# Performance work log

Hardware: AMD Instinct MI355X
Metric: run time of the kernel (lower is better)

The kernel has to match this reference:

```python
import jax, jax.numpy as jnp
import numpy as np

H1 = 768
H2 = 768
B, LQ, LK = 8, 1024, 1024


def setup_inputs() -> dict:
    key = jax.random.key(0)
    ks = jax.random.split(key, 12)
    s1 = 1.0 / np.sqrt(H1)
    s2 = 1.0 / np.sqrt(H2)
    # weights stored as [in, out] (equivalent to torch Linear weight.T)
    return {
        "tensor1": jax.random.normal(ks[0], (B, LQ, H1), jnp.float32),
        "tensor2": jax.random.normal(ks[1], (B, LK, H2), jnp.float32),
        "Wq": jax.random.uniform(ks[2], (3, H1, H2), jnp.float32, -s1, s1),
        "bq": jax.random.uniform(ks[3], (3, H2), jnp.float32, -s1, s1),
        "Wk": jax.random.uniform(ks[4], (3, H2, H2), jnp.float32, -s2, s2),
        "bk": jax.random.uniform(ks[5], (3, H2), jnp.float32, -s2, s2),
        "Wv": jax.random.uniform(ks[6], (3, H2, H2), jnp.float32, -s2, s2),
        "bv": jax.random.uniform(ks[7], (3, H2), jnp.float32, -s2, s2),
        "Wp": jax.random.uniform(ks[8], (3 * H2, H2), jnp.float32, -1.0 / np.sqrt(3 * H2), 1.0 / np.sqrt(3 * H2)),
        "bp": jax.random.uniform(ks[9], (H2,), jnp.float32, -1.0 / np.sqrt(3 * H2), 1.0 / np.sqrt(3 * H2)),
    }


def reference(tensor1, tensor2, Wq, bq, Wk, bk, Wv, bv, Wp, bp):
    # Three independent cross-attention heads, stacked on leading axis h=3.
    q = jnp.einsum("bqd,hde->hbqe", tensor1, Wq) + bq[:, None, None, :]  # [3,B,LQ,H2]
    k = jnp.einsum("bkd,hde->hbke", tensor2, Wk) + bk[:, None, None, :]  # [3,B,LK,H2]
    v = jnp.einsum("bkd,hde->hbke", tensor2, Wv) + bv[:, None, None, :]  # [3,B,LK,H2]
    scores = jnp.einsum("hbqe,hbke->hbqk", q, k)  # NOTE: no 1/sqrt(d) scaling, per original
    weights = jax.nn.softmax(scores, axis=-1)
    ctx = jnp.einsum("hbqk,hbke->hbqe", weights, v)  # [3,B,LQ,H2]
    # concat heads along feature dim -> [B,LQ,3*H2]
    multi = jnp.transpose(ctx, (1, 2, 0, 3)).reshape(ctx.shape[1], ctx.shape[2], -1)
    # project_multihead: ReLU then Linear
    return jax.nn.relu(multi) @ Wp + bp
```

## Files before the change

### kernel.cpp

```cpp
#include <hip/hip_runtime.h>
#include <hip/hip_bf16.h>


typedef _Float16 f16;
typedef __attribute__((ext_vector_type(8))) _Float16 f16x8;
typedef __attribute__((ext_vector_type(4))) float f32x4;
typedef __attribute__((ext_vector_type(4))) short s16x4;

#define DI __device__ __forceinline__

DI short f2hs(float f){
  f16 h = (f16)f;
  return __builtin_bit_cast(short, h);
}
DI float hs2f(short s){
  return (float)__builtin_bit_cast(f16, s);
}

DI f32x4 mfma16(f16x8 a, f16x8 b, f32x4 c){
  return __builtin_amdgcn_mfma_f32_16x16x32_f16(a, b, c, 0, 0, 0);
}

#define GLL16(gp, lp) __builtin_amdgcn_global_load_lds( \
    (const __attribute__((address_space(1))) unsigned int*)(gp), \
    (__attribute__((address_space(3))) unsigned int*)(lp), 16, 0, 0)

__global__ void cvt2_f16_kernel(const float* __restrict__ a, const float* __restrict__ b,
                                short* __restrict__ oa, short* __restrict__ ob, int n4each){
  int i = blockIdx.x * blockDim.x + threadIdx.x;
  const float* in = (i < n4each) ? a : b;
  short* out = (i < n4each) ? oa : ob;
  int j = (i < n4each) ? i : i - n4each;
  f32x4 v = ((const f32x4*)in)[j];
  s16x4 o;
  o[0]=f2hs(v[0]); o[1]=f2hs(v[1]); o[2]=f2hs(v[2]); o[3]=f2hs(v[3]);
  ((s16x4*)out)[j] = o;
}

__global__ void transpose2_kernel(const float* __restrict__ Wv, const float* __restrict__ Wp,
                                  short* __restrict__ WvT, short* __restrict__ WpT){
  __shared__ float tile[32][33];
  const float* in; short* out; int R, r0;
  if (blockIdx.z == 0){
    int hd = blockIdx.y / 24;
    in = Wv + (long)hd*768*768; out = WvT + (long)hd*768*768;
    R = 768; r0 = (blockIdx.y % 24) * 32;
  } else {
    in = Wp; out = WpT; R = 2304; r0 = blockIdx.y * 32;
  }
  int c0 = blockIdx.x * 32;
  int tx = threadIdx.x, ty = threadIdx.y;
  #pragma unroll
  for (int k=0;k<4;k++)
    tile[ty + k*8][tx] = in[(long)(r0 + ty + k*8) * 768 + c0 + tx];
  __syncthreads();
  #pragma unroll
  for (int k=0;k<4;k++)
    out[(long)(c0 + ty + k*8) * R + r0 + tx] = f2hs(tile[tx][ty + k*8]);
}

DI void gemm_tile64(const short* __restrict__ A, const short* __restrict__ Bt, int K,
                    int m0, int n0, short* As, short* Bs, f32x4 (&acc)[4][4])
{
  const int tid = threadIdx.x, wave = tid>>6, lane = tid&63;
  const int wm = wave>>1, wn = wave&1;
  const int fl = lane&15, fq = lane>>4;
  const int srow = lane>>2, scol = (lane&3)*8;
  for (int kk=0; kk<K; kk+=64){
    __syncthreads();
    #pragma unroll
    for (int c=0;c<2;c++)
      #pragma unroll
      for (int r=0;r<2;r++){
        const int rb = r*64 + wave*16;
        GLL16(A  + (long)(m0+rb+srow)*K + kk + c*32 + scol, As + c*4096 + rb*32);
        GLL16(Bt + (long)(n0+rb+srow)*K + kk + c*32 + scol, Bs + c*4096 + rb*32);
      }
    __syncthreads();
    #pragma unroll
    for (int c=0;c<2;c++){
      f16x8 a[4];
      #pragma unroll
      for (int i=0;i<4;i++) a[i] = *(const f16x8*)(As + c*4096 + (wm*64+i*16+fl)*32 + fq*8);
      #pragma unroll
      for (int j=0;j<4;j++){
        f16x8 b = *(const f16x8*)(Bs + c*4096 + (wn*64+j*16+fl)*32 + fq*8);
        #pragma unroll
        for (int i=0;i<4;i++) acc[i][j] = mfma16(a[i], b, acc[i][j]);
      }
    }
  }
}

__global__ __launch_bounds__(256,2) void gemm_m_kernel(
    const short* __restrict__ WqH, const short* __restrict__ WkH, short* __restrict__ Mt)
{
  __shared__ short As[8192];
  __shared__ short Bs[8192];
  const int h = blockIdx.z;
  const int m0 = blockIdx.x*128, n0 = blockIdx.y*128;
  const int tid = threadIdx.x, wave = tid>>6, lane = tid&63;
  const int wm = wave>>1, wn = wave&1;
  const int fl = lane&15, fq = lane>>4;

  f32x4 vz = {0.f,0.f,0.f,0.f};
  f32x4 acc[4][4];
  #pragma unroll
  for (int i=0;i<4;i++)
    #pragma unroll
    for (int j=0;j<4;j++) acc[i][j] = vz;

  gemm_tile64(WqH + (long)h*768*768, WkH + (long)h*768*768, 768, m0, n0, As, Bs, acc);

  short* outp = Mt + (long)h*768*768;
  #pragma unroll
  for (int j=0;j<4;j++){
    int col = n0 + wn*64 + j*16 + fl;
    #pragma unroll
    for (int i=0;i<4;i++){
      int row = m0 + wm*64 + i*16 + fq*4;
      s16x4 pack;
      #pragma unroll
      for (int r=0;r<4;r++) pack[r] = f2hs(acc[i][j][r]);
      *(s16x4*)(outp + (long)col*768 + row) = pack;
    }
  }
}

__global__ void vvec_kernel(const float* __restrict__ Wk, const float* __restrict__ bq,
                            float* __restrict__ w){
  const int h = blockIdx.x, chunk = blockIdx.y;
  const int tid = threadIdx.x, wave = tid>>6, lane = tid&63;
  const float* bql = bq + h*768 + lane*12;
  float bv[12];
  #pragma unroll
  for (int e=0;e<12;e++) bv[e] = bql[e];
  for (int r = 0; r < 24; r++){
    int d = chunk*96 + r*4 + wave;
    const float* row = Wk + ((long)h*768 + d)*768 + lane*12;
    float s = 0.f;
    #pragma unroll
    for (int e=0;e<12;e++) s += row[e] * bv[e];
    s += __shfl_xor(s, 1);
    s += __shfl_xor(s, 2);
    s += __shfl_xor(s, 4);
    s += __shfl_xor(s, 8);
    s += __shfl_xor(s, 16);
    s += __shfl_xor(s, 32);
    if (lane == 0) w[h*768 + d] = s;
  }
}

__global__ __launch_bounds__(512,2) void gemm_gv256_kernel(
    const short* __restrict__ t1b, const short* __restrict__ t2b,
    const short* __restrict__ Mt, const short* __restrict__ WvT,
    const float* __restrict__ wv, const float* __restrict__ bv,
    short* __restrict__ Gb, short* __restrict__ Vtb)
{
  __shared__ short As4[4][8192];
  __shared__ short Bs4[4][8192];

  const int z = blockIdx.z;
  const int h = z % 3, which = z / 3;
  const short* A  = (which==0) ? t1b : t2b;
  const short* Bt = ((which==0)?Mt:WvT) + (long)h*768*768;
  const int m0 = blockIdx.x*256, n0 = blockIdx.y*256;
  const int tid = threadIdx.x, wave = tid>>6, lane = tid&63;
  const int wm = wave>>2, wn = wave&3;
  const int fl = lane&15, fq = lane>>4;

  const int lr = lane>>2;
  const int ss = ((lane&3) ^ ((lane>>3)&3)) * 8;
  const int rs = (fq ^ ((fl>>1)&3)) * 8;

  f32x4 vz = {0.f,0.f,0.f,0.f};
  f32x4 acc[8][4];
  #pragma unroll
  for (int i=0;i<8;i++)
    #pragma unroll
    for (int j=0;j<4;j++) acc[i][j] = vz;

  auto STAGE = [&](int rg, int s){
    const int kk = s*32;
    #pragma unroll
    for (int g=0; g<2; g++){
      const int rb = g*128 + wave*16;
      GLL16(A  + (long)(m0+rb+lr)*768 + kk + ss, &As4[rg][rb*32]);
      GLL16(Bt + (long)(n0+rb+lr)*768 + kk + ss, &Bs4[rg][rb*32]);
    }
  };

  auto COMPUTE = [&](int rg){
    const short* Ab = &As4[rg][0];
    const short* Bb = &Bs4[rg][0];
    f16x8 b[4];
    #pragma unroll
    for (int j=0;j<4;j++)
      b[j] = *(const f16x8*)(Bb + (wn*64 + j*16 + fl)*32 + rs);
    #pragma unroll
    for (int mq=0; mq<2; mq++){
      f16x8 a[4];
      #pragma unroll
      for (int i=0;i<4;i++)
        a[i] = *(const f16x8*)(Ab + (wm*128 + mq*64 + i*16 + fl)*32 + rs);
      __builtin_amdgcn_s_setprio(1);
      #pragma unroll
      for (int j=0;j<4;j++)
        #pragma unroll
        for (int i=0;i<4;i++)
          acc[mq*4+i][j] = mfma16(a[i], b[j], acc[mq*4+i][j]);
      __builtin_amdgcn_s_setprio(0);
    }
  };

  STAGE(0, 0);
  STAGE(1, 1);
  asm volatile("s_waitcnt vmcnt(4)" ::: "memory");
  __builtin_amdgcn_s_barrier();

  for (int s = 0; s < 22; ++s){
    STAGE((s+2)&3, s+2);
    asm volatile("s_waitcnt vmcnt(8)" ::: "memory");
    __builtin_amdgcn_s_barrier();
    COMPUTE(s&3);
  }
  asm volatile("s_waitcnt vmcnt(4)" ::: "memory");
  __builtin_amdgcn_s_barrier();
  COMPUTE(22&3);
  asm volatile("s_waitcnt vmcnt(0)" ::: "memory");
  __builtin_amdgcn_s_barrier();
  COMPUTE(23&3);

  if (which == 0){
    const float* bias = wv + h*768;
    short* outp = Gb + (long)h*8192*768;
    #pragma unroll
    for (int j=0;j<4;j++){
      int col = n0 + wn*64 + j*16 + fl;
      float bb = bias[col];
      #pragma unroll
      for (int i=0;i<8;i++){
        int row = m0 + wm*128 + i*16 + fq*4;
        #pragma unroll
        for (int r=0;r<4;r++)
          outp[(long)(row+r)*768 + col] = f2hs(acc[i][j][r] + bb);
      }
    }
  } else {
    const float* bias = bv + h*768;
    const int bidx = m0 >> 10;
    const int lk0  = m0 & 1023;
    short* outp = Vtb + (long)(h*8 + bidx)*768*1024;
    #pragma unroll
    for (int j=0;j<4;j++){
      int e = n0 + wn*64 + j*16 + fl;
      float bb = bias[e];
      #pragma unroll
      for (int i=0;i<8;i++){
        int lk = lk0 + wm*128 + i*16 + fq*4;
        s16x4 pack;
        #pragma unroll
        for (int r=0;r<4;r++) pack[r] = f2hs(acc[i][j][r] + bb);
        *(s16x4*)(outp + (long)e*1024 + lk) = pack;
      }
    }
  }
}

__global__ __launch_bounds__(256,2) void qk_exp_kernel(
    const short* __restrict__ Gb, const short* __restrict__ t2b,
    short* __restrict__ P, float* __restrict__ Mx, float* __restrict__ Lx)
{
  __shared__ short As[8192];
  __shared__ short Bs[8192];
  __shared__ float red0[2][2][64];
  __shared__ float red1[2][2][64];
  const int id = blockIdx.x;
  const int xcd = id & 7, s_ = id >> 3;
  const int hb = xcd*3 + (s_ >> 6);
  const int inner = s_ & 63;
  const int qt = inner & 7, ct = inner >> 3;
  const int h = hb >> 3, b = hb & 7;
  const int tid = threadIdx.x, wave = tid>>6, lane = tid&63;
  const int wm = wave>>1, wn = wave&1;
  const int fl = lane&15, fq = lane>>4;
  const short* Abase = Gb + ((long)h*8192 + b*1024)*768;
  const short* Bbase = t2b + (long)b*1024*768;

  f32x4 vz = {0.f,0.f,0.f,0.f};
  f32x4 acc[4][4];
  #pragma unroll
  for (int i=0;i<4;i++)
    #pragma unroll
    for (int j=0;j<4;j++) acc[i][j] = vz;

  gemm_tile64(Abase, Bbase, 768, qt*128, ct*128, As, Bs, acc);

  float mt[4][4];
  #pragma unroll
  for (int i=0;i<4;i++)
    #pragma unroll
    for (int r=0;r<4;r++){
      float m = acc[i][0][r];
      #pragma unroll
      for (int j=1;j<4;j++) m = fmaxf(m, acc[i][j][r]);
      m = fmaxf(m, __shfl_xor(m, 1));
      m = fmaxf(m, __shfl_xor(m, 2));
      m = fmaxf(m, __shfl_xor(m, 4));
      m = fmaxf(m, __shfl_xor(m, 8));
      mt[i][r] = m;
      if (fl == 0) red0[wn][wm][i*16 + fq*4 + r] = m;
    }
  __syncthreads();
  #pragma unroll
  for (int i=0;i<4;i++)
    #pragma unroll
    for (int r=0;r<4;r++)
      mt[i][r] = fmaxf(red0[0][wm][i*16 + fq*4 + r], red0[1][wm][i*16 + fq*4 + r]);

  #pragma unroll
  for (int i=0;i<4;i++)
    #pragma unroll
    for (int r=0;r<4;r++){
      float s = 0.f;
      #pragma unroll
      for (int j=0;j<4;j++){
        float p = __expf(acc[i][j][r] - mt[i][r]);
        acc[i][j][r] = p;
        s += p;
      }
      s += __shfl_xor(s, 1);
      s += __shfl_xor(s, 2);
      s += __shfl_xor(s, 4);
      s += __shfl_xor(s, 8);
      if (fl == 0) red1[wn][wm][i*16 + fq*4 + r] = s;
    }
  __syncthreads();

  #pragma unroll
  for (int j=0;j<4;j++){
    int c = ct*128 + wn*64 + j*16 + fl;
    #pragma unroll
    for (int i=0;i<4;i++){
      int q = qt*128 + wm*64 + i*16 + fq*4;
      #pragma unroll
      for (int r=0;r<4;r++)
        P[((long)hb*1024 + q + r)*1024 + c] = f2hs(acc[i][j][r]);
    }
  }
  if (fl == 0 && wn == 0){
    long aux = ((long)(hb*8 + ct))*1024 + qt*128;
    #pragma unroll
    for (int i=0;i<4;i++)
      #pragma unroll
      for (int r=0;r<4;r++){
        int row = wm*64 + i*16 + fq*4 + r;
        Mx[aux + row] = mt[i][r];
        Lx[aux + row] = red1[0][wm][row & 63] + red1[1][wm][row & 63];
      }
  }
}

__global__ __launch_bounds__(256,2) void pv_kernel(
    const short* __restrict__ P, const short* __restrict__ Vtb,
    const float* __restrict__ Mx, const float* __restrict__ Lx, short* __restrict__ multi)
{
  __shared__ short As[8192];
  __shared__ short Bs[8192];
  __shared__ float scl[8][128];
  const int id = blockIdx.x;
  const int xcd = id & 7, s_ = id >> 3;
  const int hb = xcd*3 + s_/48;
  const int inner = s_ % 48;
  const int qt = inner & 7, et = inner >> 3;
  const int h = hb >> 3, b = hb & 7;
  const int tid = threadIdx.x, wave = tid>>6, lane = tid&63;
  const int wm = wave>>1, wn = wave&1;
  const int fl = lane&15, fq = lane>>4;
  const int srow = lane>>2, scol = (lane&3)*8;
  const short* Abase = P + (long)hb*1024*1024 + (long)(qt*128)*1024;
  const short* Bbase = Vtb + (long)hb*768*1024 + (long)(et*128)*1024;

  if (tid < 128){
    long a0 = ((long)(hb*8))*1024 + qt*128 + tid;
    float m[8], l[8];
    #pragma unroll
    for (int t=0;t<8;t++){ m[t] = Mx[a0 + t*1024]; l[t] = Lx[a0 + t*1024]; }
    float mg = m[0];
    #pragma unroll
    for (int t=1;t<8;t++) mg = fmaxf(mg, m[t]);
    float lg = 0.f;
    #pragma unroll
    for (int t=0;t<8;t++) lg += l[t] * __expf(m[t] - mg);
    float inv = 1.0f / lg;
    #pragma unroll
    for (int t=0;t<8;t++) scl[t][tid] = __expf(m[t] - mg) * inv;
  }
  __syncthreads();

  f32x4 vz = {0.f,0.f,0.f,0.f};
  f32x4 acc[4][4];
  #pragma unroll
  for (int i=0;i<4;i++)
    #pragma unroll
    for (int j=0;j<4;j++) acc[i][j] = vz;

  for (int ct=0; ct<8; ct++){
    f16 s[4];
    #pragma unroll
    for (int i=0;i<4;i++) s[i] = (f16)scl[ct][wm*64 + i*16 + fl];
    #pragma unroll
    for (int t=0;t<2;t++){
      const int kk = ct*128 + t*64;
      __syncthreads();
      #pragma unroll
      for (int c=0;c<2;c++)
        #pragma unroll
        for (int r=0;r<2;r++){
          const int rb = r*64 + wave*16;
          GLL16(Abase + (long)(rb+srow)*1024 + kk + c*32 + scol, As + c*4096 + rb*32);
          GLL16(Bbase + (long)(rb+srow)*1024 + kk + c*32 + scol, Bs + c*4096 + rb*32);
        }
      __syncthreads();
      #pragma unroll
      for (int c=0;c<2;c++){
        f16x8 a[4];
        #pragma unroll
        for (int i=0;i<4;i++){
          f16x8 av = *(const f16x8*)(As + c*4096 + (wm*64+i*16+fl)*32 + fq*8);
          f16x8 sv;
          #pragma unroll
          for (int e=0;e<8;e++) sv[e] = s[i];
          a[i] = av * sv;
        }
        #pragma unroll
        for (int j=0;j<4;j++){
          f16x8 bvv = *(const f16x8*)(Bs + c*4096 + (wn*64+j*16+fl)*32 + fq*8);
          #pragma unroll
          for (int i=0;i<4;i++) acc[i][j] = mfma16(a[i], bvv, acc[i][j]);
        }
      }
    }
  }

  short* mp = multi + (long)(b*1024 + qt*128)*2304 + h*768 + et*128;
  #pragma unroll
  for (int j=0;j<4;j++){
    int e = wn*64 + j*16 + fl;
    #pragma unroll
    for (int i=0;i<4;i++){
      int q = wm*64 + i*16 + fq*4;
      #pragma unroll
      for (int r=0;r<4;r++)
        mp[(long)(q+r)*2304 + e] = f2hs(fmaxf(acc[i][j][r], 0.f));
    }
  }
}

__global__ __launch_bounds__(256,2) void gemm_out_kernel(
    const short* __restrict__ A, const short* __restrict__ Bt,
    const float* __restrict__ bias, float* __restrict__ out)
{
  __shared__ short As[8192];
  __shared__ short Bs[8192];
  const int m0 = blockIdx.x*128, n0 = blockIdx.y*128;
  const int tid = threadIdx.x, wave = tid>>6, lane = tid&63;
  const int wm = wave>>1, wn = wave&1;
  const int fl = lane&15, fq = lane>>4;

  f32x4 vz = {0.f,0.f,0.f,0.f};
  f32x4 acc[4][4];
  #pragma unroll
  for (int i=0;i<4;i++)
    #pragma unroll
    for (int j=0;j<4;j++) acc[i][j] = vz;

  gemm_tile64(A, Bt, 2304, m0, n0, As, Bs, acc);

  #pragma unroll
  for (int j=0;j<4;j++){
    int col = n0 + wn*64 + j*16 + fl;
    float bb = bias[col];
    #pragma unroll
    for (int i=0;i<4;i++){
      int row = m0 + wm*64 + i*16 + fq*4;
      #pragma unroll
      for (int r=0;r<4;r++)
        out[(long)(row+r)*768 + col] = acc[i][j][r] + bb;
    }
  }
}

extern "C" void kernel_launch(void* const* d_in, const int* in_sizes, int n_in,
                              void* d_out, int out_size, void* d_ws, size_t ws_size,
                              hipStream_t stream)
{
  const float* t1 = (const float*)d_in[0];
  const float* t2 = (const float*)d_in[1];
  const float* Wq = (const float*)d_in[2];
  const float* bq = (const float*)d_in[3];
  const float* Wk = (const float*)d_in[4];
  const float* Wv = (const float*)d_in[6];
  const float* bv = (const float*)d_in[7];
  const float* Wp = (const float*)d_in[8];
  const float* bp = (const float*)d_in[9];
  float* out = (float*)d_out;

  char* ws = (char*)d_ws;
  size_t off = 0;
  auto carve = [&](size_t bytes){ void* p = ws + off; off += (bytes + 255) & ~(size_t)255; return p; };
  short* t1b = (short*)carve(8L*1024*768*2);
  short* t2b = (short*)carve(8L*1024*768*2);
  short* WqH = (short*)carve(3L*768*768*2);
  short* WkH = (short*)carve(3L*768*768*2);
  short* WvT = (short*)carve(3L*768*768*2);
  short* WpT = (short*)carve(768L*2304*2);
  short* Mt  = (short*)carve(3L*768*768*2);
  short* Gb  = (short*)carve(3L*8192*768*2);
  short* Vtb = (short*)carve(3L*8*768*1024*2);
  short* Pb  = (short*)carve(24L*1024*1024*2);
  float* Mx  = (float*)carve(24L*8*1024*4);
  float* Lx  = (float*)carve(24L*8*1024*4);
  float* wvb = (float*)carve(3L*768*4);
  short* multib = Gb;

  cvt2_f16_kernel<<<12288, 256, 0, stream>>>(t1, t2, t1b, t2b, 1572864);
  cvt2_f16_kernel<<<3456, 256, 0, stream>>>(Wq, Wk, WqH, WkH, 442368);
  transpose2_kernel<<<dim3(24,72,2), dim3(32,8), 0, stream>>>(Wv, Wp, WvT, WpT);
  vvec_kernel<<<dim3(3,8), 256, 0, stream>>>(Wk, bq, wvb);
  gemm_m_kernel<<<dim3(6,6,3), 256, 0, stream>>>(WqH, WkH, Mt);
  gemm_gv256_kernel<<<dim3(32,3,6), 512, 0, stream>>>(t1b, t2b, Mt, WvT, wvb, bv, Gb, Vtb);
  qk_exp_kernel<<<1536, 256, 0, stream>>>(Gb, t2b, Pb, Mx, Lx);
  pv_kernel<<<1152, 256, 0, stream>>>(Pb, Vtb, Mx, Lx, multib);
  gemm_out_kernel<<<dim3(64,6,1), 256, 0, stream>>>(multib, WpT, bp, out);
}
```

Before: 413.3 us.

## Deepen GEMM prefetch pipeline with register double-buffered fragments and merged head grid

The G/V projection GEMM now treats the three heads as one wide N dimension (grid 32x9x2 instead of 32x3x6) and precomputes base global pointers. The main loop is restructured to keep three stages of LDS loads in flight instead of two. LDS fragment reads for the next step are double-buffered in registers and issued after the MFMA block, so LDS latency overlaps compute with a single barrier per k-step. The aim is to hide memory and LDS latency better, at the cost of more VGPR pressure from the extra fragment buffers and a fully unrolled loop.

```diff
diff --git a/kernel.cpp b/kernel.cpp
--- a/kernel.cpp
+++ b/kernel.cpp
@@ -151,7 +151,7 @@
   }
 }
 
-__global__ __launch_bounds__(512,2) void gemm_gv256_kernel(
+__global__ __launch_bounds__(512,2) void gemm_gv2_kernel(
     const short* __restrict__ t1b, const short* __restrict__ t2b,
     const short* __restrict__ Mt, const short* __restrict__ WvT,
     const float* __restrict__ wv, const float* __restrict__ bv,
@@ -160,10 +160,9 @@
   __shared__ short As4[4][8192];
   __shared__ short Bs4[4][8192];
 
-  const int z = blockIdx.z;
-  const int h = z % 3, which = z / 3;
-  const short* A  = (which==0) ? t1b : t2b;
-  const short* Bt = ((which==0)?Mt:WvT) + (long)h*768*768;
+  const int which = blockIdx.z;
+  const short* A  = which ? t2b : t1b;
+  const short* Bt = which ? WvT : Mt;
   const int m0 = blockIdx.x*256, n0 = blockIdx.y*256;
   const int tid = threadIdx.x, wave = tid>>6, lane = tid&63;
   const int wm = wave>>2, wn = wave&3;
@@ -173,6 +172,9 @@
   const int ss = ((lane&3) ^ ((lane>>3)&3)) * 8;
   const int rs = (fq ^ ((fl>>1)&3)) * 8;
 
+  const short* Agl = A  + (long)(m0+lr)*768 + ss;
+  const short* Bgl = Bt + (long)(n0+lr)*768 + ss;
+
   f32x4 vz = {0.f,0.f,0.f,0.f};
   f32x4 acc[8][4];
   #pragma unroll
@@ -180,87 +182,95 @@
     #pragma unroll
     for (int j=0;j<4;j++) acc[i][j] = vz;
 
-  auto STAGE = [&](int rg, int s){
+  auto STAGE = [&](int sl, int s){
     const int kk = s*32;
     #pragma unroll
     for (int g=0; g<2; g++){
       const int rb = g*128 + wave*16;
-      GLL16(A  + (long)(m0+rb+lr)*768 + kk + ss, &As4[rg][rb*32]);
-      GLL16(Bt + (long)(n0+rb+lr)*768 + kk + ss, &Bs4[rg][rb*32]);
+      GLL16(Agl + (long)rb*768 + kk, &As4[sl][rb*32]);
+      GLL16(Bgl + (long)rb*768 + kk, &Bs4[sl][rb*32]);
     }
   };
 
-  auto COMPUTE = [&](int rg){
-    const short* Ab = &As4[rg][0];
-    const short* Bb = &Bs4[rg][0];
-    f16x8 b[4];
-    #pragma unroll
-    for (int j=0;j<4;j++)
-      b[j] = *(const f16x8*)(Bb + (wn*64 + j*16 + fl)*32 + rs);
-    #pragma unroll
-    for (int mq=0; mq<2; mq++){
-      f16x8 a[4];
-      #pragma unroll
-      for (int i=0;i<4;i++)
-        a[i] = *(const f16x8*)(Ab + (wm*128 + mq*64 + i*16 + fl)*32 + rs);
-      __builtin_amdgcn_s_setprio(1);
-      #pragma unroll
-      for (int j=0;j<4;j++)
-        #pragma unroll
-        for (int i=0;i<4;i++)
-          acc[mq*4+i][j] = mfma16(a[i], b[j], acc[mq*4+i][j]);
-      __builtin_amdgcn_s_setprio(0);
-    }
+  f16x8 a1[2][4], bb[2][4], a2[4];
+
+  auto READN = [&](int nx, int sl){
+    const short* Ab = &As4[sl][0];
+    const short* Bb = &Bs4[sl][0];
+    #pragma unroll
+    for (int j=0;j<4;j++) bb[nx][j] = *(const f16x8*)(Bb + (wn*64 + j*16 + fl)*32 + rs);
+    #pragma unroll
+    for (int i=0;i<4;i++) a1[nx][i] = *(const f16x8*)(Ab + (wm*128 + i*16 + fl)*32 + rs);
   };
 
   STAGE(0, 0);
   STAGE(1, 1);
-  asm volatile("s_waitcnt vmcnt(4)" ::: "memory");
-  __builtin_amdgcn_s_barrier();
-
-  for (int s = 0; s < 22; ++s){
-    STAGE((s+2)&3, s+2);
-    asm volatile("s_waitcnt vmcnt(8)" ::: "memory");
-    __builtin_amdgcn_s_barrier();
-    COMPUTE(s&3);
-  }
-  asm volatile("s_waitcnt vmcnt(4)" ::: "memory");
-  __builtin_amdgcn_s_barrier();
-  COMPUTE(22&3);
-  asm volatile("s_waitcnt vmcnt(0)" ::: "memory");
-  __builtin_amdgcn_s_barrier();
-  COMPUTE(23&3);
-
+  STAGE(2, 2);
+  asm volatile("s_waitcnt vmcnt(8)" ::: "memory");
+  asm volatile("s_barrier" ::: "memory");
+  READN(0, 0);
+
+  #pragma unroll
+  for (int s = 0; s < 24; ++s){
+    const int cur = s&1, nxt = cur^1;
+    if (s <= 20) STAGE((s+3)&3, s+3);
+    if (s <= 20)      asm volatile("s_waitcnt vmcnt(8)" ::: "memory");
+    else if (s == 21) asm volatile("s_waitcnt vmcnt(4)" ::: "memory");
+    else if (s == 22) asm volatile("s_waitcnt vmcnt(0)" ::: "memory");
+    {
+      const short* Ab = &As4[s&3][0];
+      #pragma unroll
+      for (int i=0;i<4;i++)
+        a2[i] = *(const f16x8*)(Ab + (wm*128 + 64 + i*16 + fl)*32 + rs);
+    }
+    __builtin_amdgcn_s_setprio(1);
+    #pragma unroll
+    for (int j=0;j<4;j++)
+      #pragma unroll
+      for (int i=0;i<4;i++)
+        acc[i][j] = mfma16(a1[cur][i], bb[cur][j], acc[i][j]);
+    #pragma unroll
+    for (int j=0;j<4;j++)
+      #pragma unroll
+      for (int i=0;i<4;i++)
+        acc[4+i][j] = mfma16(a2[i], bb[cur][j], acc[4+i][j]);
+    __builtin_amdgcn_s_setprio(0);
+    asm volatile("s_barrier" ::: "memory");
+    if (s < 23) READN(nxt, (s+1)&3);
+  }
+
+  const int hN = n0 / 768;
+  const int e0 = n0 - hN*768;
   if (which == 0){
-    const float* bias = wv + h*768;
-    short* outp = Gb + (long)h*8192*768;
+    short* outp = Gb + (long)hN*8192*768;
     #pragma unroll
     for (int j=0;j<4;j++){
-      int col = n0 + wn*64 + j*16 + fl;
-      float bb = bias[col];
+      int cg  = n0 + wn*64 + j*16 + fl;
+      int col = e0 + wn*64 + j*16 + fl;
+      float bb_ = wv[cg];
       #pragma unroll
       for (int i=0;i<8;i++){
-        int row = m0 + wm*128 + i*16 + fq*4;
+        int row = m0 + wm*128 + (i/4)*64 + (i%4)*16 + fq*4;
         #pragma unroll
         for (int r=0;r<4;r++)
-          outp[(long)(row+r)*768 + col] = f2hs(acc[i][j][r] + bb);
+          outp[(long)(row+r)*768 + col] = f2hs(acc[i][j][r] + bb_);
       }
     }
   } else {
-    const float* bias = bv + h*768;
     const int bidx = m0 >> 10;
     const int lk0  = m0 & 1023;
-    short* outp = Vtb + (long)(h*8 + bidx)*768*1024;
+    short* outp = Vtb + (long)(hN*8 + bidx)*768*1024;
     #pragma unroll
     for (int j=0;j<4;j++){
-      int e = n0 + wn*64 + j*16 + fl;
-      float bb = bias[e];
+      int cg = n0 + wn*64 + j*16 + fl;
+      int e  = e0 + wn*64 + j*16 + fl;
+      float bb_ = bv[cg];
       #pragma unroll
       for (int i=0;i<8;i++){
-        int lk = lk0 + wm*128 + i*16 + fq*4;
+        int lk = lk0 + wm*128 + (i/4)*64 + (i%4)*16 + fq*4;
         s16x4 pack;
         #pragma unroll
-        for (int r=0;r<4;r++) pack[r] = f2hs(acc[i][j][r] + bb);
+        for (int r=0;r<4;r++) pack[r] = f2hs(acc[i][j][r] + bb_);
         *(s16x4*)(outp + (long)e*1024 + lk) = pack;
       }
     }
@@ -529,7 +539,7 @@
   transpose2_kernel<<<dim3(24,72,2), dim3(32,8), 0, stream>>>(Wv, Wp, WvT, WpT);
   vvec_kernel<<<dim3(3,8), 256, 0, stream>>>(Wk, bq, wvb);
   gemm_m_kernel<<<dim3(6,6,3), 256, 0, stream>>>(WqH, WkH, Mt);
-  gemm_gv256_kernel<<<dim3(32,3,6), 512, 0, stream>>>(t1b, t2b, Mt, WvT, wvb, bv, Gb, Vtb);
+  gemm_gv2_kernel<<<dim3(32,9,2), 512, 0, stream>>>(t1b, t2b, Mt, WvT, wvb, bv, Gb, Vtb);
   qk_exp_kernel<<<1536, 256, 0, stream>>>(Gb, t2b, Pb, Mx, Lx);
   pv_kernel<<<1152, 256, 0, stream>>>(Pb, Vtb, Mx, Lx, multib);
   gemm_out_kernel<<<dim3(64,6,1), 256, 0, stream>>>(multib, WpT, bp, out);
```

Measured after the change: 423.0 us. 1.02x slower.
